# Performance work log

Hardware: AMD Instinct MI355X
Metric: run time of the kernel (lower is better)

## Reference

```python
import jax, jax.numpy as jnp
import numpy as np

B, N, D, H, DH = 2, 2048, 1024, 16, 64
SCALE = DH ** -0.5


def setup_inputs() -> dict:
    key = jax.random.key(0)
    k1, k2, k3 = jax.random.split(key, 3)
    x = jax.random.normal(k1, (B, N, D), dtype=jnp.float32)
    w_qkv = jax.random.normal(k2, (D, 3 * H * DH), dtype=jnp.float32) * 0.02
    w_out = jax.random.normal(k3, (H * DH, D), dtype=jnp.float32) * 0.02
    # causal boolean mask, broadcast over (b, h)
    attn_mask = jnp.tril(jnp.ones((N, N), dtype=bool))
    return {"x": x, "attn_mask": attn_mask, "w_qkv": w_qkv, "w_out": w_out}


def reference(x, attn_mask, w_qkv, w_out):
    b, n, _ = x.shape
    # fused QKV projection; Rearrange 'b n (qkv h d) -> qkv b h n d'
    qkv = (x @ w_qkv).reshape(b, n, 3, H, DH)
    qkv = jnp.transpose(qkv, (2, 0, 3, 1, 4))  # [3, b, h, n, d]
    q, k, v = qkv[0], qkv[1], qkv[2]
    q = q * SCALE
    sim = jnp.einsum('bhid,bhjd->bhij', q, k)  # [b, h, n, n]
    neg = -jnp.finfo(sim.dtype).max
    sim = jnp.where(attn_mask, sim, neg)
    attn = jax.nn.softmax(sim, axis=-1)
    out = jnp.einsum('bhij,bhjd->bhid', attn, v)  # [b, h, n, d]
    out = jnp.transpose(out, (0, 2, 1, 3)).reshape(b, n, H * DH)
    return out @ w_out
```

## Files before the change

kernel.cpp:

```cpp
#include <hip/hip_runtime.h>
#include <hip/hip_bf16.h>


typedef unsigned short u16;
typedef unsigned int u32;
typedef __bf16 bf16x8 __attribute__((ext_vector_type(8)));
typedef float  f32x4  __attribute__((ext_vector_type(4)));
typedef unsigned short u16x4 __attribute__((ext_vector_type(4)));

#define DEV __device__ __forceinline__

DEV float exp2fast(float x) { return __builtin_amdgcn_exp2f(x); }

DEV u16 f2bf(float f) {
  unsigned u = __builtin_bit_cast(unsigned, f);
  return (u16)((u + 0x7FFFu + ((u >> 16) & 1u)) >> 16);
}

DEV f32x4 mfma16(bf16x8 a, bf16x8 b, f32x4 c) {
  return __builtin_amdgcn_mfma_f32_16x16x32_bf16(a, b, c, 0, 0, 0);
}

template <typename T>
DEV void gload16(const T* g, T* l) {
  __builtin_amdgcn_global_load_lds((__attribute__((address_space(1))) void*)g,
                                   (__attribute__((address_space(3))) void*)l, 16, 0, 0);
}


__global__ __launch_bounds__(256) void cvt_x(const float* __restrict__ x,
                                             u16* __restrict__ xb) {
  int idx = (blockIdx.x * 256 + threadIdx.x) * 4;
  float4 v = *(const float4*)(x + idx);
  u16x4 u = { f2bf(v.x), f2bf(v.y), f2bf(v.z), f2bf(v.w) };
  *(u16x4*)(xb + idx) = u;
}

__global__ __launch_bounds__(256) void wtrans(const float* __restrict__ src,
                                              u16* __restrict__ dst,
                                              int R, int C, int scaleLim) {
  __shared__ u16 T[64][72];
  const int tid = threadIdx.x;
  const int c0 = blockIdx.x * 64, r0 = blockIdx.y * 64;
  const int cl = tid & 63;
  const float scale = (c0 + cl < scaleLim) ? 0.125f * 1.4426950408889634f : 1.0f;
#pragma unroll
  for (int i = 0; i < 16; ++i) {
    int r = (tid >> 6) * 16 + i;
    T[cl][r] = f2bf(src[(size_t)(r0 + r) * C + c0 + cl] * scale);
  }
  __syncthreads();
#pragma unroll
  for (int i = 0; i < 16; ++i) {
    int cc = (tid >> 6) * 16 + i;
    dst[(size_t)(c0 + cc) * R + r0 + cl] = T[cc][cl];
  }
}

__global__ __launch_bounds__(256) void vtrans(const u16* __restrict__ qkv,
                                              u16* __restrict__ vtout) {
  __shared__ u16 T[64][72];
  const int tid = threadIdx.x;
  const int n0 = blockIdx.x * 64;
  const int h = blockIdx.y, b = blockIdx.z;
  const int dl = tid & 63;
#pragma unroll
  for (int i = 0; i < 16; ++i) {
    int n = (tid >> 6) * 16 + i;
    T[dl][n] = qkv[(size_t)(b * 2048 + n0 + n) * 3072 + 2048 + h * 64 + dl];
  }
  __syncthreads();
#pragma unroll
  for (int i = 0; i < 16; ++i) {
    int d = (tid >> 6) * 16 + i;
    vtout[(size_t)((b * 16 + h) * 64 + d) * 2048 + n0 + dl] = T[d][dl];
  }
}


__global__ __launch_bounds__(256) void gemm_bf16(const u16* __restrict__ A,
                                                 const u16* __restrict__ Bt,
                                                 u16* __restrict__ Cb,
                                                 int N, int nx, int cpx) {
  __shared__ __align__(16) u16 lA[128 * 64];
  __shared__ __align__(16) u16 lB[128 * 64];
  const int tid = threadIdx.x;
  const int lane = tid & 63, w = tid >> 6;
  const int g = lane >> 4, r16 = lane & 15;
  const int wm = w >> 1, wn = w & 1;
  const int id = (int)blockIdx.x;
  const int newid = (id & 7) * cpx + (id >> 3);
  const int m0 = (newid / nx) * 128, n0 = (newid % nx) * 128;

  const f32x4 z4 = {0.f, 0.f, 0.f, 0.f};
  f32x4 acc[4][4];
#pragma unroll
  for (int m = 0; m < 4; ++m)
#pragma unroll
    for (int n = 0; n < 4; ++n) acc[m][n] = z4;

  for (int kt = 0; kt < 16; ++kt) {
    const int kbase = kt * 64;
#pragma unroll
    for (int issue = 0; issue < 4; ++issue) {
      int i = issue * 256 + tid;
      int r = i >> 3, jp = (i & 7) ^ (r & 7);
      gload16(A + (size_t)(m0 + r) * 1024 + kbase + jp * 8,
              lA + (size_t)(issue * 256 + (tid & ~63)) * 8);
      gload16(Bt + (size_t)(n0 + r) * 1024 + kbase + jp * 8,
              lB + (size_t)(issue * 256 + (tid & ~63)) * 8);
    }
    __syncthreads();
#pragma unroll
    for (int kk = 0; kk < 2; ++kk) {
      bf16x8 a[4], b[4];
#pragma unroll
      for (int m = 0; m < 4; ++m) {
        int row = wm * 64 + m * 16 + r16;
        int off = row * 128 + ((kk * 64 + g * 16) ^ ((r16 & 7) << 4));
        a[m] = *(const bf16x8*)((const char*)lA + off);
      }
#pragma unroll
      for (int n = 0; n < 4; ++n) {
        int row = wn * 64 + n * 16 + r16;
        int off = row * 128 + ((kk * 64 + g * 16) ^ ((r16 & 7) << 4));
        b[n] = *(const bf16x8*)((const char*)lB + off);
      }
      __builtin_amdgcn_s_setprio(1);
#pragma unroll
      for (int m = 0; m < 4; ++m)
#pragma unroll
        for (int n = 0; n < 4; ++n) acc[m][n] = mfma16(a[m], b[n], acc[m][n]);
      __builtin_amdgcn_s_setprio(0);
    }
    __syncthreads();
  }
#pragma unroll
  for (int m = 0; m < 4; ++m)
#pragma unroll
    for (int n = 0; n < 4; ++n) {
      int col = n0 + wn * 64 + n * 16 + r16;
#pragma unroll
      for (int j = 0; j < 4; ++j) {
        int row = m0 + wm * 64 + m * 16 + g * 4 + j;
        Cb[(size_t)row * N + col] = f2bf(acc[m][n][j]);
      }
    }
}


__global__ __launch_bounds__(256) void gemm64(const u16* __restrict__ A,
                                              const u16* __restrict__ Bt,
                                              float* __restrict__ Cf,
                                              int N, int nx, int cpx) {
  __shared__ __align__(16) u16 lA[64 * 64];
  __shared__ __align__(16) u16 lB[64 * 64];
  const int tid = threadIdx.x;
  const int lane = tid & 63, w = tid >> 6;
  const int g = lane >> 4, r16 = lane & 15;
  const int wm = w >> 1, wn = w & 1;
  const int id = (int)blockIdx.x;
  const int newid = (id & 7) * cpx + (id >> 3);
  const int m0 = (newid / nx) * 64, n0 = (newid % nx) * 64;

  const f32x4 z4 = {0.f, 0.f, 0.f, 0.f};
  f32x4 acc[2][2];
#pragma unroll
  for (int m = 0; m < 2; ++m)
#pragma unroll
    for (int n = 0; n < 2; ++n) acc[m][n] = z4;

  for (int kt = 0; kt < 16; ++kt) {
    const int kbase = kt * 64;
#pragma unroll
    for (int issue = 0; issue < 2; ++issue) {
      int i = issue * 256 + tid;
      int r = i >> 3, jp = (i & 7) ^ (r & 7);
      gload16(A + (size_t)(m0 + r) * 1024 + kbase + jp * 8,
              lA + (size_t)(issue * 256 + (tid & ~63)) * 8);
      gload16(Bt + (size_t)(n0 + r) * 1024 + kbase + jp * 8,
              lB + (size_t)(issue * 256 + (tid & ~63)) * 8);
    }
    __syncthreads();
#pragma unroll
    for (int kk = 0; kk < 2; ++kk) {
      bf16x8 a[2], b[2];
#pragma unroll
      for (int m = 0; m < 2; ++m) {
        int row = wm * 32 + m * 16 + r16;
        int off = row * 128 + ((kk * 64 + g * 16) ^ ((r16 & 7) << 4));
        a[m] = *(const bf16x8*)((const char*)lA + off);
      }
#pragma unroll
      for (int n = 0; n < 2; ++n) {
        int row = wn * 32 + n * 16 + r16;
        int off = row * 128 + ((kk * 64 + g * 16) ^ ((r16 & 7) << 4));
        b[n] = *(const bf16x8*)((const char*)lB + off);
      }
      __builtin_amdgcn_s_setprio(1);
#pragma unroll
      for (int m = 0; m < 2; ++m)
#pragma unroll
        for (int n = 0; n < 2; ++n) acc[m][n] = mfma16(a[m], b[n], acc[m][n]);
      __builtin_amdgcn_s_setprio(0);
    }
    __syncthreads();
  }
#pragma unroll
  for (int m = 0; m < 2; ++m)
#pragma unroll
    for (int n = 0; n < 2; ++n) {
      int col = n0 + wn * 32 + n * 16 + r16;
#pragma unroll
      for (int j = 0; j < 4; ++j) {
        int row = m0 + wm * 32 + m * 16 + g * 4 + j;
        Cf[(size_t)row * N + col] = acc[m][n][j];
      }
    }
}


__global__ __launch_bounds__(256) void attn_fused(const u16* __restrict__ qkv,
                                                  const u16* __restrict__ vt,
                                                  u16* __restrict__ ao) {
  __shared__ __align__(16) u16 lK[2][64 * 64];
  __shared__ __align__(16) u16 lV[2][64 * 64];
  __shared__ __align__(16) u16 lP[4][16 * 64];
  const int tid = threadIdx.x;
  const int lane = tid & 63, w = tid >> 6;
  const int g = lane >> 4, r16 = lane & 15;

  const int flat = (int)blockIdx.x;
  const int xcd = flat & 7;
  const int cu = (flat >> 3) & 31;
  const int round = (flat >> 8) & 3;
  const int grp = xcd * 4 + round;
  const int qt = (round & 1) ? cu : 31 - cu;
  const int b = grp >> 4, h = grp & 15;
  const int q0w = qt * 64 + w * 16;

  bf16x8 aq[2];
  {
    const u16* qrow = qkv + (size_t)(b * 2048 + q0w + r16) * 3072 + h * 64;
    aq[0] = *(const bf16x8*)(qrow + g * 8);
    aq[1] = *(const bf16x8*)(qrow + 32 + g * 8);
  }

  const int r = tid >> 3, jp = (tid & 7) ^ (r & 7);
  const u16* ksrc = qkv + (size_t)(b * 2048 + r) * 3072 + 1024 + h * 64 + jp * 8;
  const u16* vsrc = vt + (size_t)((b * 16 + h) * 64 + r) * 2048 + jp * 8;
  const size_t ldst = (size_t)(tid & ~63) * 8;

  const f32x4 z4 = {0.f, 0.f, 0.f, 0.f};
  f32x4 o[4];
#pragma unroll
  for (int n = 0; n < 4; ++n) o[n] = z4;
  float mrun = -INFINITY, lrun = 0.f;

  gload16(ksrc, lK[0] + ldst);
  gload16(ksrc + (size_t)32 * 3072, lK[0] + 2048 + ldst);
  gload16(vsrc, lV[0] + ldst);
  gload16(vsrc + (size_t)32 * 2048, lV[0] + 2048 + ldst);
  __syncthreads();

  int cur = 0;
  u16* lp = lP[w];
  for (int t = 0; t <= qt; ++t) {
    if (t < qt) {
      const u16* kn = ksrc + (size_t)(t + 1) * 64 * 3072;
      const u16* vn = vsrc + (size_t)(t + 1) * 64;
      gload16(kn, lK[cur ^ 1] + ldst);
      gload16(kn + (size_t)32 * 3072, lK[cur ^ 1] + 2048 + ldst);
      gload16(vn, lV[cur ^ 1] + ldst);
      gload16(vn + (size_t)32 * 2048, lV[cur ^ 1] + 2048 + ldst);
    }
    f32x4 s[4];
#pragma unroll
    for (int f = 0; f < 4; ++f) s[f] = z4;
    __builtin_amdgcn_s_setprio(1);
#pragma unroll
    for (int kk = 0; kk < 2; ++kk) {
#pragma unroll
      for (int f = 0; f < 4; ++f) {
        int row = f * 16 + r16;
        int off = row * 128 + ((kk * 64 + g * 16) ^ ((r16 & 7) << 4));
        bf16x8 ak = *(const bf16x8*)((const char*)lK[cur] + off);
        s[f] = mfma16(ak, aq[kk], s[f]);
      }
    }
    __builtin_amdgcn_s_setprio(0);
    if (t == qt) {
      const int qrel = w * 16 + r16;
#pragma unroll
      for (int f = 0; f < 4; ++f)
#pragma unroll
        for (int j = 0; j < 4; ++j)
          if (f * 16 + g * 4 + j > qrel) s[f][j] = -3.0e38f;
    }
    float mx = fmaxf(fmaxf(fmaxf(s[0][0], s[0][1]), fmaxf(s[0][2], s[0][3])),
                     fmaxf(fmaxf(s[1][0], s[1][1]), fmaxf(s[1][2], s[1][3])));
    mx = fmaxf(mx, fmaxf(fmaxf(fmaxf(s[2][0], s[2][1]), fmaxf(s[2][2], s[2][3])),
                         fmaxf(fmaxf(s[3][0], s[3][1]), fmaxf(s[3][2], s[3][3]))));
    mx = fmaxf(mx, __shfl_xor(mx, 16));
    mx = fmaxf(mx, __shfl_xor(mx, 32));
    if (!__all(mx - mrun <= 8.0f)) {
      float mnew = fmaxf(mrun, mx);
      float corr = exp2fast(mrun - mnew);
      mrun = mnew;
      lrun *= corr;
      float cj[4];
#pragma unroll
      for (int j = 0; j < 4; ++j) cj[j] = __shfl(corr, g * 4 + j);
#pragma unroll
      for (int n = 0; n < 4; ++n)
#pragma unroll
        for (int j = 0; j < 4; ++j) o[n][j] *= cj[j];
    }
    float sm = 0.f;
#pragma unroll
    for (int f = 0; f < 4; ++f)
#pragma unroll
      for (int j = 0; j < 4; ++j) {
        s[f][j] = exp2fast(s[f][j] - mrun);
        sm += s[f][j];
      }
    sm += __shfl_xor(sm, 16);
    sm += __shfl_xor(sm, 32);
    lrun += sm;

#pragma unroll
    for (int f = 0; f < 4; ++f) {
      u32 w0 = (u32)f2bf(s[f][0]) | ((u32)f2bf(s[f][1]) << 16);
      u32 w1 = (u32)f2bf(s[f][2]) | ((u32)f2bf(s[f][3]) << 16);
      int base = r16 * 128 + ((f * 32 + g * 8) ^ ((r16 & 7) << 4));
      *(u32*)((char*)lp + base) = w0;
      *(u32*)((char*)lp + base + 4) = w1;
    }
    __builtin_amdgcn_s_setprio(1);
#pragma unroll
    for (int ks = 0; ks < 2; ++ks) {
      int abyte = r16 * 128 + ((ks * 64 + g * 16) ^ ((r16 & 7) << 4));
      bf16x8 ap = *(const bf16x8*)((const char*)lp + abyte);
#pragma unroll
      for (int n = 0; n < 4; ++n) {
        int row = n * 16 + r16;
        int off = row * 128 + ((ks * 64 + g * 16) ^ ((r16 & 7) << 4));
        bf16x8 bv = *(const bf16x8*)((const char*)lV[cur] + off);
        o[n] = mfma16(ap, bv, o[n]);
      }
    }
    __builtin_amdgcn_s_setprio(0);
    __syncthreads();
    cur ^= 1;
  }
  float lj[4];
#pragma unroll
  for (int j = 0; j < 4; ++j) lj[j] = __shfl(lrun, g * 4 + j);
#pragma unroll
  for (int n = 0; n < 4; ++n) {
    int col = h * 64 + n * 16 + r16;
#pragma unroll
    for (int j = 0; j < 4; ++j) {
      int row = b * 2048 + q0w + g * 4 + j;
      ao[(size_t)row * 1024 + col] = f2bf(o[n][j] * (1.f / lj[j]));
    }
  }
}


extern "C" void kernel_launch(void* const* d_in, const int* in_sizes, int n_in,
                              void* d_out, int out_size, void* d_ws, size_t ws_size,
                              hipStream_t stream) {
  const float* x     = (const float*)d_in[0];
  const float* w_qkv = (const float*)d_in[2];
  const float* w_out = (const float*)d_in[3];
  float* out = (float*)d_out;

  u16* ws = (u16*)d_ws;
  u16* x_bf  = ws;
  u16* wqkvT = x_bf + (size_t)4096 * 1024;
  u16* woutT = wqkvT + (size_t)3072 * 1024;
  u16* qkv   = woutT + (size_t)1024 * 1024;
  u16* ao    = qkv + (size_t)4096 * 3072;
  u16* vtb   = x_bf;

  cvt_x<<<4096, 256, 0, stream>>>(x, x_bf);
  wtrans<<<dim3(48, 16), 256, 0, stream>>>(w_qkv, wqkvT, 1024, 3072, 1024);
  wtrans<<<dim3(16, 16), 256, 0, stream>>>(w_out, woutT, 1024, 1024, 0);
  gemm_bf16<<<768, 256, 0, stream>>>(x_bf, wqkvT, qkv, 3072, 24, 96);
  vtrans<<<dim3(32, 16, 2), 256, 0, stream>>>(qkv, vtb);
  attn_fused<<<1024, 256, 0, stream>>>(qkv, vtb, ao);
  gemm64<<<1024, 256, 0, stream>>>(ao, woutT, out, 1024, 16, 128);
}
```

Baseline: 195.2 us.

## Fuse V transpose into QKV GEMM epilogue and keep P in registers

The QKV GEMM epilogue now writes Q/K to a compact buffer and V directly in transposed layout, which removes the separate vtrans kernel and its extra global round trip. The attention kernel permutes the K row loading so the score MFMA output lanes already match the A-operand layout for the PV MFMA. That lets the probabilities feed the MFMA straight from registers instead of going through an LDS scratch buffer. The two weight transposes are also merged into one launch. The cost is a more intricate index mapping for K rows and the causal mask, plus scattered 8-byte transposed stores in the GEMM epilogue.

```diff
diff --git a/kernel.cpp b/kernel.cpp
--- a/kernel.cpp
+++ b/kernel.cpp
@@ -7,6 +7,7 @@
 typedef __bf16 bf16x8 __attribute__((ext_vector_type(8)));
 typedef float  f32x4  __attribute__((ext_vector_type(4)));
 typedef unsigned short u16x4 __attribute__((ext_vector_type(4)));
+typedef unsigned int u32x4 __attribute__((ext_vector_type(4)));
 
 #define DEV __device__ __forceinline__
 
@@ -36,14 +37,19 @@
   *(u16x4*)(xb + idx) = u;
 }
 
-__global__ __launch_bounds__(256) void wtrans(const float* __restrict__ src,
-                                              u16* __restrict__ dst,
-                                              int R, int C, int scaleLim) {
+__global__ __launch_bounds__(256) void wtrans_all(const float* __restrict__ wq,
+                                                  const float* __restrict__ wo,
+                                                  u16* __restrict__ dq,
+                                                  u16* __restrict__ dow) {
   __shared__ u16 T[64][72];
   const int tid = threadIdx.x;
-  const int c0 = blockIdx.x * 64, r0 = blockIdx.y * 64;
+  int bx = blockIdx.x;
+  const float* src; u16* dst; int C, sl;
+  if (bx < 48) { src = wq; dst = dq; C = 3072; sl = 1024; }
+  else         { bx -= 48; src = wo; dst = dow; C = 1024; sl = 0; }
+  const int c0 = bx * 64, r0 = blockIdx.y * 64;
   const int cl = tid & 63;
-  const float scale = (c0 + cl < scaleLim) ? 0.125f * 1.4426950408889634f : 1.0f;
+  const float scale = (c0 + cl < sl) ? 0.125f * 1.4426950408889634f : 1.0f;
 #pragma unroll
   for (int i = 0; i < 16; ++i) {
     int r = (tid >> 6) * 16 + i;
@@ -53,35 +59,16 @@
 #pragma unroll
   for (int i = 0; i < 16; ++i) {
     int cc = (tid >> 6) * 16 + i;
-    dst[(size_t)(c0 + cc) * R + r0 + cl] = T[cc][cl];
-  }
-}
-
-__global__ __launch_bounds__(256) void vtrans(const u16* __restrict__ qkv,
-                                              u16* __restrict__ vtout) {
-  __shared__ u16 T[64][72];
-  const int tid = threadIdx.x;
-  const int n0 = blockIdx.x * 64;
-  const int h = blockIdx.y, b = blockIdx.z;
-  const int dl = tid & 63;
-#pragma unroll
-  for (int i = 0; i < 16; ++i) {
-    int n = (tid >> 6) * 16 + i;
-    T[dl][n] = qkv[(size_t)(b * 2048 + n0 + n) * 3072 + 2048 + h * 64 + dl];
-  }
-  __syncthreads();
-#pragma unroll
-  for (int i = 0; i < 16; ++i) {
-    int d = (tid >> 6) * 16 + i;
-    vtout[(size_t)((b * 16 + h) * 64 + d) * 2048 + n0 + dl] = T[d][dl];
+    dst[(size_t)(c0 + cc) * 1024 + r0 + cl] = T[cc][cl];
   }
 }
 
 
 __global__ __launch_bounds__(256) void gemm_bf16(const u16* __restrict__ A,
                                                  const u16* __restrict__ Bt,
-                                                 u16* __restrict__ Cb,
-                                                 int N, int nx, int cpx) {
+                                                 u16* __restrict__ qk,
+                                                 u16* __restrict__ vt,
+                                                 int nx, int cpx) {
   __shared__ __align__(16) u16 lA[128 * 64];
   __shared__ __align__(16) u16 lB[128 * 64];
   const int tid = threadIdx.x;
@@ -135,17 +122,33 @@
     }
     __syncthreads();
   }
-#pragma unroll
-  for (int m = 0; m < 4; ++m)
-#pragma unroll
-    for (int n = 0; n < 4; ++n) {
-      int col = n0 + wn * 64 + n * 16 + r16;
-#pragma unroll
-      for (int j = 0; j < 4; ++j) {
-        int row = m0 + wm * 64 + m * 16 + g * 4 + j;
-        Cb[(size_t)row * N + col] = f2bf(acc[m][n][j]);
-      }
-    }
+  if (n0 < 2048) {
+#pragma unroll
+    for (int m = 0; m < 4; ++m)
+#pragma unroll
+      for (int n = 0; n < 4; ++n) {
+        int col = n0 + wn * 64 + n * 16 + r16;
+#pragma unroll
+        for (int j = 0; j < 4; ++j) {
+          int row = m0 + wm * 64 + m * 16 + g * 4 + j;
+          qk[(size_t)row * 2048 + col] = f2bf(acc[m][n][j]);
+        }
+      }
+  } else {
+#pragma unroll
+    for (int m = 0; m < 4; ++m) {
+      int row0 = m0 + wm * 64 + m * 16 + g * 4;
+      int b = row0 >> 11, nn0 = row0 & 2047;
+#pragma unroll
+      for (int n = 0; n < 4; ++n) {
+        int hcol = n0 - 2048 + wn * 64 + n * 16 + r16;
+        int h = hcol >> 6, d = hcol & 63;
+        u16x4 pk = { f2bf(acc[m][n][0]), f2bf(acc[m][n][1]),
+                     f2bf(acc[m][n][2]), f2bf(acc[m][n][3]) };
+        *(u16x4*)(vt + (size_t)((b * 16 + h) * 64 + d) * 2048 + nn0) = pk;
+      }
+    }
+  }
 }
 
 
@@ -220,12 +223,11 @@
 }
 
 
-__global__ __launch_bounds__(256) void attn_fused(const u16* __restrict__ qkv,
+__global__ __launch_bounds__(256) void attn_fused(const u16* __restrict__ qk,
                                                   const u16* __restrict__ vt,
                                                   u16* __restrict__ ao) {
   __shared__ __align__(16) u16 lK[2][64 * 64];
   __shared__ __align__(16) u16 lV[2][64 * 64];
-  __shared__ __align__(16) u16 lP[4][16 * 64];
   const int tid = threadIdx.x;
   const int lane = tid & 63, w = tid >> 6;
   const int g = lane >> 4, r16 = lane & 15;
@@ -241,13 +243,14 @@
 
   bf16x8 aq[2];
   {
-    const u16* qrow = qkv + (size_t)(b * 2048 + q0w + r16) * 3072 + h * 64;
+    const u16* qrow = qk + (size_t)(b * 2048 + q0w + r16) * 2048 + h * 64;
     aq[0] = *(const bf16x8*)(qrow + g * 8);
     aq[1] = *(const bf16x8*)(qrow + 32 + g * 8);
   }
 
   const int r = tid >> 3, jp = (tid & 7) ^ (r & 7);
-  const u16* ksrc = qkv + (size_t)(b * 2048 + r) * 3072 + 1024 + h * 64 + jp * 8;
+  const int rp = (r & 0x23) | ((r & 0x0C) << 1) | ((r & 0x10) >> 2);
+  const u16* ksrc = qk + (size_t)(b * 2048 + rp) * 2048 + 1024 + h * 64 + jp * 8;
   const u16* vsrc = vt + (size_t)((b * 16 + h) * 64 + r) * 2048 + jp * 8;
   const size_t ldst = (size_t)(tid & ~63) * 8;
 
@@ -258,19 +261,18 @@
   float mrun = -INFINITY, lrun = 0.f;
 
   gload16(ksrc, lK[0] + ldst);
-  gload16(ksrc + (size_t)32 * 3072, lK[0] + 2048 + ldst);
+  gload16(ksrc + (size_t)32 * 2048, lK[0] + 2048 + ldst);
   gload16(vsrc, lV[0] + ldst);
   gload16(vsrc + (size_t)32 * 2048, lV[0] + 2048 + ldst);
   __syncthreads();
 
   int cur = 0;
-  u16* lp = lP[w];
   for (int t = 0; t <= qt; ++t) {
     if (t < qt) {
-      const u16* kn = ksrc + (size_t)(t + 1) * 64 * 3072;
+      const u16* kn = ksrc + (size_t)(t + 1) * 64 * 2048;
       const u16* vn = vsrc + (size_t)(t + 1) * 64;
       gload16(kn, lK[cur ^ 1] + ldst);
-      gload16(kn + (size_t)32 * 3072, lK[cur ^ 1] + 2048 + ldst);
+      gload16(kn + (size_t)32 * 2048, lK[cur ^ 1] + 2048 + ldst);
       gload16(vn, lV[cur ^ 1] + ldst);
       gload16(vn + (size_t)32 * 2048, lV[cur ^ 1] + 2048 + ldst);
     }
@@ -294,8 +296,10 @@
 #pragma unroll
       for (int f = 0; f < 4; ++f)
 #pragma unroll
-        for (int j = 0; j < 4; ++j)
-          if (f * 16 + g * 4 + j > qrel) s[f][j] = -3.0e38f;
+        for (int j = 0; j < 4; ++j) {
+          int kvt = (f >> 1) * 32 + g * 8 + (f & 1) * 4 + j;
+          if (kvt > qrel) s[f][j] = -3.0e38f;
+        }
     }
     float mx = fmaxf(fmaxf(fmaxf(s[0][0], s[0][1]), fmaxf(s[0][2], s[0][3])),
                      fmaxf(fmaxf(s[1][0], s[1][1]), fmaxf(s[1][2], s[1][3])));
@@ -328,19 +332,17 @@
     sm += __shfl_xor(sm, 32);
     lrun += sm;
 
+    u32 pa[8];
 #pragma unroll
     for (int f = 0; f < 4; ++f) {
-      u32 w0 = (u32)f2bf(s[f][0]) | ((u32)f2bf(s[f][1]) << 16);
-      u32 w1 = (u32)f2bf(s[f][2]) | ((u32)f2bf(s[f][3]) << 16);
-      int base = r16 * 128 + ((f * 32 + g * 8) ^ ((r16 & 7) << 4));
-      *(u32*)((char*)lp + base) = w0;
-      *(u32*)((char*)lp + base + 4) = w1;
+      pa[f * 2 + 0] = (u32)f2bf(s[f][0]) | ((u32)f2bf(s[f][1]) << 16);
+      pa[f * 2 + 1] = (u32)f2bf(s[f][2]) | ((u32)f2bf(s[f][3]) << 16);
     }
     __builtin_amdgcn_s_setprio(1);
 #pragma unroll
     for (int ks = 0; ks < 2; ++ks) {
-      int abyte = r16 * 128 + ((ks * 64 + g * 16) ^ ((r16 & 7) << 4));
-      bf16x8 ap = *(const bf16x8*)((const char*)lp + abyte);
+      u32x4 pav = { pa[ks * 4 + 0], pa[ks * 4 + 1], pa[ks * 4 + 2], pa[ks * 4 + 3] };
+      bf16x8 ap = __builtin_bit_cast(bf16x8, pav);
 #pragma unroll
       for (int n = 0; n < 4; ++n) {
         int row = n * 16 + r16;
@@ -380,15 +382,13 @@
   u16* x_bf  = ws;
   u16* wqkvT = x_bf + (size_t)4096 * 1024;
   u16* woutT = wqkvT + (size_t)3072 * 1024;
-  u16* qkv   = woutT + (size_t)1024 * 1024;
-  u16* ao    = qkv + (size_t)4096 * 3072;
-  u16* vtb   = x_bf;
+  u16* qk    = woutT + (size_t)1024 * 1024;
+  u16* vtb   = qk + (size_t)4096 * 2048;
+  u16* ao    = vtb + (size_t)2048 * 2048;
 
   cvt_x<<<4096, 256, 0, stream>>>(x, x_bf);
-  wtrans<<<dim3(48, 16), 256, 0, stream>>>(w_qkv, wqkvT, 1024, 3072, 1024);
-  wtrans<<<dim3(16, 16), 256, 0, stream>>>(w_out, woutT, 1024, 1024, 0);
-  gemm_bf16<<<768, 256, 0, stream>>>(x_bf, wqkvT, qkv, 3072, 24, 96);
-  vtrans<<<dim3(32, 16, 2), 256, 0, stream>>>(qkv, vtb);
-  attn_fused<<<1024, 256, 0, stream>>>(qkv, vtb, ao);
+  wtrans_all<<<dim3(64, 16), 256, 0, stream>>>(w_qkv, w_out, wqkvT, woutT);
+  gemm_bf16<<<768, 256, 0, stream>>>(x_bf, wqkvT, qk, vtb, 24, 96);
+  attn_fused<<<1024, 256, 0, stream>>>(qk, vtb, ao);
   gemm64<<<1024, 256, 0, stream>>>(ao, woutT, out, 1024, 16, 128);
 }
```

After: 198.7 us. Within noise of the previous version (+1.8%).
